# Optimization experiments

Measured on AMD Instinct MI355X. Metric: run time of the kernel, lower is better.

Reference implementation:

```python
import jax, jax.numpy as jnp
import numpy as np

NUM_HEADS = 8
H_SCALE = 1000.0
WIND_THRESHOLD = 5.0


def setup_inputs() -> dict:
    key = jax.random.key(0)
    ks = jax.random.split(key, 8)
    B, N, C = 8, 1024, 256
    H = W = 64  # (H//2)*(W//2) == N
    x = jax.random.normal(ks[0], (B, N, C), dtype=jnp.float32)
    elevation = jax.random.uniform(ks[1], (B, N), dtype=jnp.float32)
    u_wind = jax.random.normal(ks[2], (B, H, W), dtype=jnp.float32)
    v_wind = jax.random.normal(ks[3], (B, H, W), dtype=jnp.float32)
    w_qkv = jax.random.normal(ks[4], (3 * C, C), dtype=jnp.float32) * (C ** -0.5)
    w_proj = jax.random.normal(ks[5], (C, C), dtype=jnp.float32) * (C ** -0.5)
    b_proj = jnp.zeros((C,), dtype=jnp.float32)
    alpha = jnp.float32(1.0)
    beta = jnp.float32(0.3)
    return {"x": x, "elevation": elevation, "u_wind": u_wind, "v_wind": v_wind,
            "w_qkv": w_qkv, "w_proj": w_proj, "b_proj": b_proj,
            "alpha": alpha, "beta": beta}


def _wind_strength(u_wind, v_wind):
    # 2x2 average pool of wind magnitude -> [B, N]
    B, H, W = u_wind.shape
    mag = jnp.sqrt(u_wind ** 2 + v_wind ** 2 + 1e-8)
    mag = mag.reshape(B, H // 2, 2, W // 2, 2).mean(axis=(2, 4))
    return mag.reshape(B, -1)


def _elevation_bias(elevation, u_wind, v_wind, alpha, beta):
    # elev_diff[b,i,j] = elev[b,j] - elev[b,i]
    elev_diff = elevation[:, None, :] - elevation[:, :, None]
    bias = -alpha * jax.nn.relu(elev_diff / H_SCALE)
    ws = _wind_strength(u_wind, v_wind)  # [B, N]
    wind_factor = jax.nn.sigmoid((ws[:, None, :] + ws[:, :, None]) * 0.5 - WIND_THRESHOLD)
    bias = bias * (1.0 - beta * wind_factor)
    return jnp.clip(bias, -10.0, 0.0)  # [B, N, N]


def reference(x, elevation, u_wind, v_wind, w_qkv, w_proj, b_proj, alpha, beta):
    B, N, C = x.shape
    hd = C // NUM_HEADS
    scale = hd ** -0.5
    qkv = (x @ w_qkv.T).reshape(B, N, 3, NUM_HEADS, hd)
    qkv = jnp.transpose(qkv, (2, 0, 3, 1, 4))  # [3, B, H, N, hd]
    q, k, v = qkv[0], qkv[1], qkv[2]
    scores = jnp.einsum('bhnd,bhmd->bhnm', q, k) * scale
    bias = _elevation_bias(elevation, u_wind, v_wind, alpha, beta)
    scores = scores + bias[:, None, :, :]
    attn = jax.nn.softmax(scores, axis=-1)
    out = jnp.einsum('bhnm,bhmd->bhnd', attn, v)
    out = jnp.transpose(out, (0, 2, 1, 3)).reshape(B, N, C)
    return out @ w_proj.T + b_proj
```

## Files before the change

kernel.cpp:

```cpp
#include <hip/hip_runtime.h>
#include <stdint.h>

typedef __attribute__((ext_vector_type(8))) short short8;
typedef __attribute__((ext_vector_type(8))) __bf16 bf16x8;
typedef __attribute__((ext_vector_type(2))) __bf16 bf16x2;
typedef __attribute__((ext_vector_type(4))) float f32x4;
typedef __attribute__((ext_vector_type(2))) unsigned int uint2_t;
typedef __attribute__((ext_vector_type(2))) float float2_t;

#define LOG2E 1.44269504f

__device__ __forceinline__ unsigned short f2bf(float f) {
  unsigned int u = __builtin_bit_cast(unsigned int, f);
  u += 0x7fffu + ((u >> 16) & 1u);
  return (unsigned short)(u >> 16);
}

__device__ __forceinline__ unsigned int pk2(float a, float b) {
  bf16x2 t;
  t[0] = (__bf16)a;
  t[1] = (__bf16)b;
  return __builtin_bit_cast(unsigned int, t);
}

__device__ __forceinline__ f32x4 mfma16(short8 a, short8 b, f32x4 c) {
  return __builtin_amdgcn_mfma_f32_16x16x32_bf16(
      __builtin_bit_cast(bf16x8, a), __builtin_bit_cast(bf16x8, b), c, 0, 0, 0);
}

__device__ __forceinline__ short8 ld8(const unsigned short* p) {
  return *reinterpret_cast<const short8*>(p);
}

__global__ __launch_bounds__(256) void k_prep(const float* __restrict__ wqkv,
                                              const float* __restrict__ wproj,
                                              const float* __restrict__ u,
                                              const float* __restrict__ v,
                                              const float* __restrict__ elev,
                                              const float* __restrict__ alphap,
                                              unsigned short* __restrict__ wqkv_bf,
                                              unsigned short* __restrict__ wproj_bf,
                                              float* __restrict__ esc,
                                              float* __restrict__ wsc) {
  int gx = blockIdx.x, t = threadIdx.x;
  if (gx < 768) {
    int i = gx * 256 + t;
    float s = (i < 256 * 256) ? (0.17677669529663687f * LOG2E) : 1.0f;
    wqkv_bf[i] = f2bf(wqkv[i] * s);
  } else if (gx < 1024) {
    int i = (gx - 768) * 256 + t;
    wproj_bf[i] = f2bf(wproj[i]);
  } else {
    int i = (gx - 1024) * 256 + t;
    int b = i >> 10, n = i & 1023;
    int ph = n >> 5, pw = n & 31;
    const float* ub = u + b * 4096;
    const float* vb = v + b * 4096;
    float s = 0.f;
#pragma unroll
    for (int dy = 0; dy < 2; ++dy)
#pragma unroll
      for (int dx = 0; dx < 2; ++dx) {
        int idx = (2 * ph + dy) * 64 + (2 * pw + dx);
        float uu = ub[idx], vv = vb[idx];
        s += sqrtf(uu * uu + vv * vv + 1e-8f);
      }
    wsc[i] = s * (0.25f * 0.5f * LOG2E);
    esc[i] = elev[i] * (alphap[0] * 1e-3f * LOG2E);
  }
}

__global__ __launch_bounds__(256, 8) void k_qkv(const float* __restrict__ x,
                                                const unsigned short* __restrict__ wq_bf,
                                                unsigned short* __restrict__ qb,
                                                unsigned short* __restrict__ kb,
                                                unsigned short* __restrict__ vT) {
  __shared__ unsigned short xs[32][264];
  const int tid = threadIdx.x;
  const int w = tid >> 6, lane = tid & 63;
  const int c = lane & 15, g = lane >> 4;
  const int wm = w & 1, wn = w >> 1;
  const int m0 = blockIdx.y * 32;
  const int n0 = blockIdx.x * 192 + wn * 96;
#pragma unroll
  for (int i = 0; i < 8; ++i) {
    int idx = i * 1024 + tid * 4;
    int row = idx >> 8, col = idx & 255;
    f32x4 vv = *reinterpret_cast<const f32x4*>(x + (size_t)(m0 + row) * 256 + col);
    uint2_t hh = {pk2(vv[0], vv[1]), pk2(vv[2], vv[3])};
    *reinterpret_cast<uint2_t*>(&xs[row][col]) = hh;
  }
  __syncthreads();
  f32x4 acc[6] = {};
#pragma unroll
  for (int k0 = 0; k0 < 256; k0 += 32) {
    short8 af = ld8(&xs[wm * 16 + c][k0 + g * 8]);
#pragma unroll
    for (int nb = 0; nb < 6; ++nb) {
      short8 bf = ld8(wq_bf + (size_t)(n0 + nb * 16 + c) * 256 + k0 + g * 8);
      acc[nb] = mfma16(af, bf, acc[nb]);
    }
  }
#pragma unroll
  for (int nb = 0; nb < 6; ++nb) {
    int col = n0 + nb * 16 + c;
    int s = col >> 8, rem = col & 255;
    int h = rem >> 5, d = rem & 31;
    int nrow0 = m0 + wm * 16 + g * 4;
    int b = nrow0 >> 10, nn = nrow0 & 1023;
    size_t bh = (size_t)(b * 8 + h);
    if (s == 2) {
      uint2_t pk = {pk2(acc[nb][0], acc[nb][1]), pk2(acc[nb][2], acc[nb][3])};
      *reinterpret_cast<uint2_t*>(vT + (bh * 32 + d) * 1024 + nn) = pk;
    } else {
      unsigned short* dst = (s == 0) ? qb : kb;
#pragma unroll
      for (int r = 0; r < 4; ++r) {
        bf16x2 one;
        one[0] = (__bf16)acc[nb][r];
        dst[(bh * 1024 + nn + r) * 32 + d] = __builtin_bit_cast(unsigned short, one[0]);
      }
    }
  }
}

__global__ __launch_bounds__(256, 4) void k_attn(const unsigned short* __restrict__ qb,
                                                 const unsigned short* __restrict__ kb,
                                                 const unsigned short* __restrict__ vT,
                                                 const float* __restrict__ esc,
                                                 const float* __restrict__ wsc,
                                                 const float* __restrict__ betap,
                                                 float* __restrict__ o_part,
                                                 float* __restrict__ ml_part) {
  __shared__ float bias_lds[32][72];
  __shared__ unsigned short p_lds[4][32][72];
  const int tid = threadIdx.x;
  const int w = tid >> 6, lane = tid & 63;
  const int c = lane & 15, g = lane >> 4;
  const int q0 = blockIdx.x * 32, b = blockIdx.y;
  const int hg = blockIdx.z & 1, sp = blockIdx.z >> 1;
  const int h = hg * 4 + w;
  const size_t bh = (size_t)(b * 8 + h);
  const int kvbase = sp * 512;
  const float beta = betap[0];

  const int sqr = tid >> 3, skv = (tid & 7) * 8;
  const float* ebs = esc + b * 1024;
  const float* wbs = wsc + b * 1024;
  const float eisc = ebs[q0 + sqr];
  const float Kw = 7.2134752f - wbs[q0 + sqr];

  auto bias_elem = [&](float ej, float wj) -> float {
    float d = fmaxf(ej - eisc, 0.f);
    float e2 = __builtin_amdgcn_exp2f(Kw - wj);
    float sig = __builtin_amdgcn_rcpf(1.0f + e2);
    float bb = d * beta * sig - d;
    return fminf(fmaxf(bb, -14.4269504f), 0.f);
  };
  auto stage_bias = [&](int kv0) {
    f32x4 ej0 = *reinterpret_cast<const f32x4*>(ebs + kv0 + skv);
    f32x4 ej1 = *reinterpret_cast<const f32x4*>(ebs + kv0 + skv + 4);
    f32x4 wj0 = *reinterpret_cast<const f32x4*>(wbs + kv0 + skv);
    f32x4 wj1 = *reinterpret_cast<const f32x4*>(wbs + kv0 + skv + 4);
    f32x4 o0, o1;
#pragma unroll
    for (int j = 0; j < 4; ++j) {
      o0[j] = bias_elem(ej0[j], wj0[j]);
      o1[j] = bias_elem(ej1[j], wj1[j]);
    }
    *reinterpret_cast<f32x4*>(&bias_lds[sqr][skv]) = o0;
    *reinterpret_cast<f32x4*>(&bias_lds[sqr][skv + 4]) = o1;
  };

  stage_bias(kvbase);

  short8 qf[2];
#pragma unroll
  for (int qs = 0; qs < 2; ++qs)
    qf[qs] = ld8(qb + (bh * 1024 + q0 + qs * 16 + c) * 32 + g * 8);

  f32x4 oacc[2][2] = {};
  float mold[2] = {-1e30f, -1e30f};
  float lrow[2] = {0.f, 0.f};
  __syncthreads();

  for (int t8 = 0; t8 < 8; ++t8) {
    const int kv0 = kvbase + t8 * 64;

    short8 kf[4];
#pragma unroll
    for (int t = 0; t < 4; ++t)
      kf[t] = ld8(kb + (bh * 1024 + kv0 + t * 16 + c) * 32 + g * 8);

#pragma unroll
    for (int qs = 0; qs < 2; ++qs) {
      f32x4 s[4];
#pragma unroll
      for (int t = 0; t < 4; ++t) {
        f32x4 bc = *reinterpret_cast<const f32x4*>(&bias_lds[qs * 16 + c][t * 16 + 4 * g]);
        s[t] = mfma16(kf[t], qf[qs], bc);
      }
      float m16 = fmaxf(fmaxf(fmaxf(s[0][0], s[0][1]), fmaxf(s[0][2], s[0][3])),
                        fmaxf(fmaxf(s[1][0], s[1][1]), fmaxf(s[1][2], s[1][3])));
      m16 = fmaxf(m16, fmaxf(fmaxf(fmaxf(s[2][0], s[2][1]), fmaxf(s[2][2], s[2][3])),
                             fmaxf(fmaxf(s[3][0], s[3][1]), fmaxf(s[3][2], s[3][3]))));
      m16 = fmaxf(m16, __shfl_xor(m16, 16));
      m16 = fmaxf(m16, __shfl_xor(m16, 32));
      if (!__all(m16 <= mold[qs] + 11.0f)) {
        float mn = fmaxf(mold[qs], m16);
        float corr = __builtin_amdgcn_exp2f(mold[qs] - mn);
        mold[qs] = mn;
        lrow[qs] *= corr;
        oacc[qs][0] *= corr;
        oacc[qs][1] *= corr;
      }
      float p[4][4];
      float ps = 0.f;
#pragma unroll
      for (int t = 0; t < 4; ++t)
#pragma unroll
        for (int r = 0; r < 4; ++r) {
          float e = __builtin_amdgcn_exp2f(s[t][r] - mold[qs]);
          p[t][r] = e;
          ps += e;
        }
      ps += __shfl_xor(ps, 16);
      ps += __shfl_xor(ps, 32);
      lrow[qs] += ps;
#pragma unroll
      for (int t = 0; t < 4; ++t) {
        uint2_t pkw = {pk2(p[t][0], p[t][1]), pk2(p[t][2], p[t][3])};
        *reinterpret_cast<uint2_t*>(&p_lds[w][qs * 16 + c][t * 16 + 4 * g]) = pkw;
      }
    }

    __syncthreads();
    if (t8 < 7) stage_bias(kv0 + 64);

#pragma unroll
    for (int t2 = 0; t2 < 2; ++t2) {
      short8 pf[2];
#pragma unroll
      for (int qs = 0; qs < 2; ++qs)
        pf[qs] = ld8(&p_lds[w][qs * 16 + c][t2 * 32 + g * 8]);
#pragma unroll
      for (int hs = 0; hs < 2; ++hs) {
        short8 vf = ld8(vT + (bh * 32 + hs * 16 + c) * 1024 + kv0 + t2 * 32 + g * 8);
#pragma unroll
        for (int qs = 0; qs < 2; ++qs)
          oacc[qs][hs] = mfma16(vf, pf[qs], oacc[qs][hs]);
      }
    }

    __syncthreads();
  }

#pragma unroll
  for (int qs = 0; qs < 2; ++qs) {
    size_t qrow = ((size_t)sp * 64 + bh) * 1024 + q0 + qs * 16 + c;
#pragma unroll
    for (int hs = 0; hs < 2; ++hs)
      *reinterpret_cast<f32x4*>(o_part + qrow * 32 + hs * 16 + 4 * g) = oacc[qs][hs];
    if (g == 0) {
      float2_t ml = {mold[qs], lrow[qs]};
      *reinterpret_cast<float2_t*>(ml_part + qrow * 2) = ml;
    }
  }
}

__global__ __launch_bounds__(256, 2) void k_proj(const float* __restrict__ o_part,
                                                 const float* __restrict__ ml_part,
                                                 const unsigned short* __restrict__ wp_bf,
                                                 const float* __restrict__ bproj,
                                                 float* __restrict__ out) {
  __shared__ unsigned short xs[32][264];
  const int tid = threadIdx.x;
  const int w = tid >> 6, lane = tid & 63;
  const int c = lane & 15, g = lane >> 4;
  const int wm = w & 1, wn = w >> 1;
  const int m0 = blockIdx.x * 32;
  const int b = m0 >> 10, q0 = m0 & 1023;

  const int qq = tid >> 3, d0 = (tid & 7) * 4;
#pragma unroll
  for (int h = 0; h < 8; ++h) {
    size_t r0 = ((size_t)(b * 8 + h) * 1024 + q0 + qq);
    size_t r1 = r0 + (size_t)64 * 1024;
    f32x4 o0 = *reinterpret_cast<const f32x4*>(o_part + r0 * 32 + d0);
    f32x4 o1 = *reinterpret_cast<const f32x4*>(o_part + r1 * 32 + d0);
    float2_t ml0 = *reinterpret_cast<const float2_t*>(ml_part + r0 * 2);
    float2_t ml1 = *reinterpret_cast<const float2_t*>(ml_part + r1 * 2);
    float mm = fmaxf(ml0[0], ml1[0]);
    float a0 = __builtin_amdgcn_exp2f(ml0[0] - mm);
    float a1 = __builtin_amdgcn_exp2f(ml1[0] - mm);
    float inv = 1.0f / (a0 * ml0[1] + a1 * ml1[1]);
    f32x4 r;
#pragma unroll
    for (int j = 0; j < 4; ++j) r[j] = (o0[j] * a0 + o1[j] * a1) * inv;
    uint2_t hh = {pk2(r[0], r[1]), pk2(r[2], r[3])};
    *reinterpret_cast<uint2_t*>(&xs[qq][h * 32 + d0]) = hh;
  }
  __syncthreads();

  f32x4 acc[8] = {};
#pragma unroll
  for (int k0 = 0; k0 < 256; k0 += 32) {
    short8 af = ld8(&xs[wm * 16 + c][k0 + g * 8]);
#pragma unroll
    for (int nb = 0; nb < 8; ++nb) {
      short8 bf = ld8(wp_bf + (size_t)(wn * 128 + nb * 16 + c) * 256 + k0 + g * 8);
      acc[nb] = mfma16(af, bf, acc[nb]);
    }
  }
#pragma unroll
  for (int nb = 0; nb < 8; ++nb) {
    int col = wn * 128 + nb * 16 + c;
    float bv = bproj[col];
#pragma unroll
    for (int r = 0; r < 4; ++r) {
      int row = m0 + wm * 16 + g * 4 + r;
      out[(size_t)row * 256 + col] = acc[nb][r] + bv;
    }
  }
}

extern "C" void kernel_launch(void* const* d_in, const int* in_sizes, int n_in,
                              void* d_out, int out_size, void* d_ws, size_t ws_size,
                              hipStream_t stream) {
  const float* x = (const float*)d_in[0];
  const float* elev = (const float*)d_in[1];
  const float* uw = (const float*)d_in[2];
  const float* vw = (const float*)d_in[3];
  const float* wqkv = (const float*)d_in[4];
  const float* wproj = (const float*)d_in[5];
  const float* bproj = (const float*)d_in[6];
  const float* alpha = (const float*)d_in[7];
  const float* beta = (const float*)d_in[8];
  float* out = (float*)d_out;

  char* p = (char*)d_ws;
  auto alloc = [&](size_t bytes) {
    char* r = p;
    p += (bytes + 255) & ~(size_t)255;
    return r;
  };
  float* esc = (float*)alloc(8192 * 4);
  float* wsc = (float*)alloc(8192 * 4);
  unsigned short* wqkv_bf = (unsigned short*)alloc((size_t)768 * 256 * 2);
  unsigned short* wproj_bf = (unsigned short*)alloc((size_t)256 * 256 * 2);
  unsigned short* qb = (unsigned short*)alloc((size_t)2097152 * 2);
  unsigned short* kb = (unsigned short*)alloc((size_t)2097152 * 2);
  unsigned short* vT = (unsigned short*)alloc((size_t)2097152 * 2);
  float* o_part = (float*)alloc((size_t)2 * 2097152 * 4);
  float* ml_part = (float*)alloc((size_t)2 * 65536 * 2 * 4);

  k_prep<<<dim3(1056), dim3(256), 0, stream>>>(wqkv, wproj, uw, vw, elev, alpha,
                                               wqkv_bf, wproj_bf, esc, wsc);
  k_qkv<<<dim3(4, 256), dim3(256), 0, stream>>>(x, wqkv_bf, qb, kb, vT);
  k_attn<<<dim3(32, 8, 4), dim3(256), 0, stream>>>(qb, kb, vT, esc, wsc, beta, o_part, ml_part);
  k_proj<<<dim3(256), dim3(256), 0, stream>>>(o_part, ml_part, wproj_bf, bproj, out);
}
```

Before: 152.4 us.

## Use 8-wave attention blocks sharing bias across heads, 4-way KV split

Measured after the change: 205.9 us. 1.35x slower.

```diff
diff --git a/kernel.cpp b/kernel.cpp
--- a/kernel.cpp
+++ b/kernel.cpp
@@ -124,7 +124,7 @@
   }
 }
 
-__global__ __launch_bounds__(256, 4) void k_attn(const unsigned short* __restrict__ qb,
+__global__ __launch_bounds__(512, 8) void k_attn(const unsigned short* __restrict__ qb,
                                                  const unsigned short* __restrict__ kb,
                                                  const unsigned short* __restrict__ vT,
                                                  const float* __restrict__ esc,
@@ -133,43 +133,35 @@
                                                  float* __restrict__ o_part,
                                                  float* __restrict__ ml_part) {
   __shared__ float bias_lds[32][72];
-  __shared__ unsigned short p_lds[4][32][72];
+  __shared__ unsigned short p_lds[8][32][40];
   const int tid = threadIdx.x;
   const int w = tid >> 6, lane = tid & 63;
   const int c = lane & 15, g = lane >> 4;
   const int q0 = blockIdx.x * 32, b = blockIdx.y;
-  const int hg = blockIdx.z & 1, sp = blockIdx.z >> 1;
-  const int h = hg * 4 + w;
-  const size_t bh = (size_t)(b * 8 + h);
-  const int kvbase = sp * 512;
+  const int sp = blockIdx.z;
+  const size_t bh = (size_t)(b * 8 + w);
+  const int kvbase = sp * 256;
   const float beta = betap[0];
 
-  const int sqr = tid >> 3, skv = (tid & 7) * 8;
+  const int sqr = tid >> 4, skv = (tid & 15) * 4;
   const float* ebs = esc + b * 1024;
   const float* wbs = wsc + b * 1024;
   const float eisc = ebs[q0 + sqr];
   const float Kw = 7.2134752f - wbs[q0 + sqr];
 
-  auto bias_elem = [&](float ej, float wj) -> float {
-    float d = fmaxf(ej - eisc, 0.f);
-    float e2 = __builtin_amdgcn_exp2f(Kw - wj);
-    float sig = __builtin_amdgcn_rcpf(1.0f + e2);
-    float bb = d * beta * sig - d;
-    return fminf(fmaxf(bb, -14.4269504f), 0.f);
-  };
   auto stage_bias = [&](int kv0) {
-    f32x4 ej0 = *reinterpret_cast<const f32x4*>(ebs + kv0 + skv);
-    f32x4 ej1 = *reinterpret_cast<const f32x4*>(ebs + kv0 + skv + 4);
-    f32x4 wj0 = *reinterpret_cast<const f32x4*>(wbs + kv0 + skv);
-    f32x4 wj1 = *reinterpret_cast<const f32x4*>(wbs + kv0 + skv + 4);
-    f32x4 o0, o1;
+    f32x4 ej = *reinterpret_cast<const f32x4*>(ebs + kv0 + skv);
+    f32x4 wj = *reinterpret_cast<const f32x4*>(wbs + kv0 + skv);
+    f32x4 o;
 #pragma unroll
     for (int j = 0; j < 4; ++j) {
-      o0[j] = bias_elem(ej0[j], wj0[j]);
-      o1[j] = bias_elem(ej1[j], wj1[j]);
-    }
-    *reinterpret_cast<f32x4*>(&bias_lds[sqr][skv]) = o0;
-    *reinterpret_cast<f32x4*>(&bias_lds[sqr][skv + 4]) = o1;
+      float d = fmaxf(ej[j] - eisc, 0.f);
+      float e2 = __builtin_amdgcn_exp2f(Kw - wj[j]);
+      float sig = __builtin_amdgcn_rcpf(1.0f + e2);
+      float bb = d * beta * sig - d;
+      o[j] = fminf(fmaxf(bb, -14.4269504f), 0.f);
+    }
+    *reinterpret_cast<f32x4*>(&bias_lds[sqr][skv]) = o;
   };
 
   stage_bias(kvbase);
@@ -184,14 +176,15 @@
   float lrow[2] = {0.f, 0.f};
   __syncthreads();
 
-  for (int t8 = 0; t8 < 8; ++t8) {
-    const int kv0 = kvbase + t8 * 64;
+  for (int t4 = 0; t4 < 4; ++t4) {
+    const int kv0 = kvbase + t4 * 64;
 
     short8 kf[4];
 #pragma unroll
     for (int t = 0; t < 4; ++t)
       kf[t] = ld8(kb + (bh * 1024 + kv0 + t * 16 + c) * 32 + g * 8);
 
+    uint2_t pq[2][4];
 #pragma unroll
     for (int qs = 0; qs < 2; ++qs) {
       f32x4 s[4];
@@ -214,35 +207,37 @@
         oacc[qs][0] *= corr;
         oacc[qs][1] *= corr;
       }
-      float p[4][4];
       float ps = 0.f;
 #pragma unroll
-      for (int t = 0; t < 4; ++t)
-#pragma unroll
-        for (int r = 0; r < 4; ++r) {
-          float e = __builtin_amdgcn_exp2f(s[t][r] - mold[qs]);
-          p[t][r] = e;
-          ps += e;
-        }
+      for (int t = 0; t < 4; ++t) {
+        float e0 = __builtin_amdgcn_exp2f(s[t][0] - mold[qs]);
+        float e1 = __builtin_amdgcn_exp2f(s[t][1] - mold[qs]);
+        float e2 = __builtin_amdgcn_exp2f(s[t][2] - mold[qs]);
+        float e3 = __builtin_amdgcn_exp2f(s[t][3] - mold[qs]);
+        ps += (e0 + e1) + (e2 + e3);
+        pq[qs][t][0] = pk2(e0, e1);
+        pq[qs][t][1] = pk2(e2, e3);
+      }
       ps += __shfl_xor(ps, 16);
       ps += __shfl_xor(ps, 32);
       lrow[qs] += ps;
-#pragma unroll
-      for (int t = 0; t < 4; ++t) {
-        uint2_t pkw = {pk2(p[t][0], p[t][1]), pk2(p[t][2], p[t][3])};
-        *reinterpret_cast<uint2_t*>(&p_lds[w][qs * 16 + c][t * 16 + 4 * g]) = pkw;
-      }
     }
 
     __syncthreads();
-    if (t8 < 7) stage_bias(kv0 + 64);
+    if (t4 < 3) stage_bias(kv0 + 64);
 
 #pragma unroll
     for (int t2 = 0; t2 < 2; ++t2) {
+#pragma unroll
+      for (int qs = 0; qs < 2; ++qs)
+#pragma unroll
+        for (int ht = 0; ht < 2; ++ht)
+          *reinterpret_cast<uint2_t*>(&p_lds[w][qs * 16 + c][ht * 16 + 4 * g]) =
+              pq[qs][2 * t2 + ht];
       short8 pf[2];
 #pragma unroll
       for (int qs = 0; qs < 2; ++qs)
-        pf[qs] = ld8(&p_lds[w][qs * 16 + c][t2 * 32 + g * 8]);
+        pf[qs] = ld8(&p_lds[w][qs * 16 + c][g * 8]);
 #pragma unroll
       for (int hs = 0; hs < 2; ++hs) {
         short8 vf = ld8(vT + (bh * 32 + hs * 16 + c) * 1024 + kv0 + t2 * 32 + g * 8);
@@ -268,57 +263,75 @@
   }
 }
 
-__global__ __launch_bounds__(256, 2) void k_proj(const float* __restrict__ o_part,
+__global__ __launch_bounds__(256, 4) void k_proj(const float* __restrict__ o_part,
                                                  const float* __restrict__ ml_part,
                                                  const unsigned short* __restrict__ wp_bf,
                                                  const float* __restrict__ bproj,
                                                  float* __restrict__ out) {
-  __shared__ unsigned short xs[32][264];
+  __shared__ unsigned short xs[16][264];
+  __shared__ float cl[8][16][4];
   const int tid = threadIdx.x;
   const int w = tid >> 6, lane = tid & 63;
   const int c = lane & 15, g = lane >> 4;
-  const int wm = w & 1, wn = w >> 1;
-  const int m0 = blockIdx.x * 32;
+  const int m0 = blockIdx.x * 16;
   const int b = m0 >> 10, q0 = m0 & 1023;
 
-  const int qq = tid >> 3, d0 = (tid & 7) * 4;
+  if (tid < 128) {
+    int h = tid >> 4, row = tid & 15;
+    size_t base = ((size_t)(b * 8 + h)) * 1024 + q0 + row;
+    float m[4], l[4];
+#pragma unroll
+    for (int s = 0; s < 4; ++s) {
+      float2_t ml = *reinterpret_cast<const float2_t*>(ml_part + (base + (size_t)s * 65536) * 2);
+      m[s] = ml[0];
+      l[s] = ml[1];
+    }
+    float mm = fmaxf(fmaxf(m[0], m[1]), fmaxf(m[2], m[3]));
+    float a[4], den = 0.f;
+#pragma unroll
+    for (int s = 0; s < 4; ++s) {
+      a[s] = __builtin_amdgcn_exp2f(m[s] - mm);
+      den += a[s] * l[s];
+    }
+    float inv = 1.0f / den;
+#pragma unroll
+    for (int s = 0; s < 4; ++s) cl[h][row][s] = a[s] * inv;
+  }
+  __syncthreads();
+
+  const int rr = tid >> 4, cs = (tid & 15) * 2;
 #pragma unroll
   for (int h = 0; h < 8; ++h) {
-    size_t r0 = ((size_t)(b * 8 + h) * 1024 + q0 + qq);
-    size_t r1 = r0 + (size_t)64 * 1024;
-    f32x4 o0 = *reinterpret_cast<const f32x4*>(o_part + r0 * 32 + d0);
-    f32x4 o1 = *reinterpret_cast<const f32x4*>(o_part + r1 * 32 + d0);
-    float2_t ml0 = *reinterpret_cast<const float2_t*>(ml_part + r0 * 2);
-    float2_t ml1 = *reinterpret_cast<const float2_t*>(ml_part + r1 * 2);
-    float mm = fmaxf(ml0[0], ml1[0]);
-    float a0 = __builtin_amdgcn_exp2f(ml0[0] - mm);
-    float a1 = __builtin_amdgcn_exp2f(ml1[0] - mm);
-    float inv = 1.0f / (a0 * ml0[1] + a1 * ml1[1]);
-    f32x4 r;
-#pragma unroll
-    for (int j = 0; j < 4; ++j) r[j] = (o0[j] * a0 + o1[j] * a1) * inv;
-    uint2_t hh = {pk2(r[0], r[1]), pk2(r[2], r[3])};
-    *reinterpret_cast<uint2_t*>(&xs[qq][h * 32 + d0]) = hh;
+    size_t base = ((size_t)(b * 8 + h)) * 1024 + q0 + rr;
+    float2_t acc2 = {0.f, 0.f};
+#pragma unroll
+    for (int s = 0; s < 4; ++s) {
+      float2_t o2 = *reinterpret_cast<const float2_t*>(o_part + (base + (size_t)s * 65536) * 32 + cs);
+      float sc = cl[h][rr][s];
+      acc2[0] += o2[0] * sc;
+      acc2[1] += o2[1] * sc;
+    }
+    *reinterpret_cast<unsigned int*>(&xs[rr][h * 32 + cs]) = pk2(acc2[0], acc2[1]);
   }
   __syncthreads();
 
-  f32x4 acc[8] = {};
+  f32x4 acc[4] = {};
 #pragma unroll
   for (int k0 = 0; k0 < 256; k0 += 32) {
-    short8 af = ld8(&xs[wm * 16 + c][k0 + g * 8]);
-#pragma unroll
-    for (int nb = 0; nb < 8; ++nb) {
-      short8 bf = ld8(wp_bf + (size_t)(wn * 128 + nb * 16 + c) * 256 + k0 + g * 8);
+    short8 af = ld8(&xs[c][k0 + g * 8]);
+#pragma unroll
+    for (int nb = 0; nb < 4; ++nb) {
+      short8 bf = ld8(wp_bf + (size_t)(w * 64 + nb * 16 + c) * 256 + k0 + g * 8);
       acc[nb] = mfma16(af, bf, acc[nb]);
     }
   }
 #pragma unroll
-  for (int nb = 0; nb < 8; ++nb) {
-    int col = wn * 128 + nb * 16 + c;
+  for (int nb = 0; nb < 4; ++nb) {
+    int col = w * 64 + nb * 16 + c;
     float bv = bproj[col];
 #pragma unroll
     for (int r = 0; r < 4; ++r) {
-      int row = m0 + wm * 16 + g * 4 + r;
+      int row = m0 + g * 4 + r;
       out[(size_t)row * 256 + col] = acc[nb][r] + bv;
     }
   }
@@ -351,12 +364,12 @@
   unsigned short* qb = (unsigned short*)alloc((size_t)2097152 * 2);
   unsigned short* kb = (unsigned short*)alloc((size_t)2097152 * 2);
   unsigned short* vT = (unsigned short*)alloc((size_t)2097152 * 2);
-  float* o_part = (float*)alloc((size_t)2 * 2097152 * 4);
-  float* ml_part = (float*)alloc((size_t)2 * 65536 * 2 * 4);
+  float* o_part = (float*)alloc((size_t)4 * 2097152 * 4);
+  float* ml_part = (float*)alloc((size_t)4 * 65536 * 2 * 4);
 
   k_prep<<<dim3(1056), dim3(256), 0, stream>>>(wqkv, wproj, uw, vw, elev, alpha,
                                                wqkv_bf, wproj_bf, esc, wsc);
   k_qkv<<<dim3(4, 256), dim3(256), 0, stream>>>(x, wqkv_bf, qb, kb, vT);
-  k_attn<<<dim3(32, 8, 4), dim3(256), 0, stream>>>(qb, kb, vT, esc, wsc, beta, o_part, ml_part);
-  k_proj<<<dim3(256), dim3(256), 0, stream>>>(o_part, ml_part, wproj_bf, bproj, out);
-}
+  k_attn<<<dim3(32, 8, 4), dim3(512), 0, stream>>>(qb, kb, vT, esc, wsc, beta, o_part, ml_part);
+  k_proj<<<dim3(512), dim3(256), 0, stream>>>(o_part, ml_part, wproj_bf, bproj, out);
+}
```
